# Kernel tuning notes

Hardware: AMD Instinct MI355X
Metric: run time of the kernel (lower is better)

## Reference

```python
import jax, jax.numpy as jnp
import numpy as np

KERNEL = 5
PAD = (KERNEL - 1) // 2  # fixed_padding with dilation=1: pad_beg = pad_end = 2


def setup_inputs() -> dict:
    key = jax.random.key(0)
    kx, kw = jax.random.split(key)
    x = jax.random.normal(kx, (4, 4, 1024, 1024), dtype=jnp.float32)
    weight = jax.random.normal(kw, (4, 4, KERNEL, KERNEL), dtype=jnp.float32)
    return {"x": x, "weight": weight}


def reference(x, weight):
    """Morphological dilation2d: out[b,o,h,w] = max_{c,i,j} (x_pad[b,c,h+i,w+j] + w[o,c,i,j]).

    Equivalent to the torch unfold + broadcast-add + max over dim C*k*k, but computed
    as a fused sliding-window max-plus without materializing the im2col tensor.
    """
    B, C, H, W = x.shape
    k = weight.shape[-1]
    xp = jnp.pad(x, ((0, 0), (0, 0), (PAD, PAD), (PAD, PAD)))  # zero pad, same as F.pad
    out = None
    for i in range(k):
        for j in range(k):
            patch = xp[:, :, i:i + H, j:j + W]          # (B, C, H, W)
            w_ij = weight[:, :, i, j]                    # (O, C)
            # max over in_channels of (x + w) for this tap
            val = jnp.max(patch[:, None] + w_ij[None, :, :, None, None], axis=2)  # (B, O, H, W)
            out = val if out is None else jnp.maximum(out, val)
    return out
```

## Files before the change

### kernel.cpp

```cpp
#include <hip/hip_runtime.h>


constexpr int Himg = 1024, Wimg = 1024, Cin = 4, Cout = 4, Kn = 5;
constexpr int TW = 128, THt = 64;
constexpr int SR = 68;
constexpr int SC4 = 34;
constexpr int S = 140;
constexpr int NCHUNK = SR * SC4;

typedef float v2f __attribute__((ext_vector_type(2)));
typedef const float __attribute__((address_space(4))) cfloat;

__device__ __forceinline__ int rot(int r) { return ((r >> 2) & 1) * 4; }

__global__ __launch_bounds__(256, 4) void morph(const float* __restrict__ x,
                                                const float* __restrict__ w,
                                                float* __restrict__ out) {
  __shared__ __align__(16) float xs[SR * S];
  const int tid = threadIdx.x;
  const int bw = blockIdx.x * TW;
  const int br = blockIdx.y * THt;
  const int b  = blockIdx.z >> 1;
  const int o0 = (blockIdx.z & 1) * 2;
  const int tx = tid & 15;
  const int ty = tid >> 4;
  const int h0 = ty * 4;
  const int w0 = tx * 8;

  cfloat* cw = (cfloat*)w;

  v2f acc[2][4][4];
#pragma unroll
  for (int oo = 0; oo < 2; ++oo)
#pragma unroll
    for (int d = 0; d < 4; ++d)
#pragma unroll
      for (int m = 0; m < 4; ++m) acc[oo][d][m] = (v2f){-3.4e38f, -3.4e38f};

#pragma unroll 1
  for (int c = 0; c < Cin; ++c) {
    if (c) __syncthreads();
    for (int idx = tid; idx < NCHUNK; idx += 256) {
      const int row = idx / SC4;
      const int ch  = idx - row * SC4;
      const int gr  = br - 2 + row;
      const int gc  = bw - 4 + ch * 4;
      float4 v = make_float4(0.f, 0.f, 0.f, 0.f);
      if ((unsigned)gr < (unsigned)Himg) {
        const float* src = x + ((size_t)(b * Cin + c) * Himg + gr) * Wimg;
        if (gc >= 0 && gc <= Wimg - 4) {
          v = *(const float4*)(src + gc);
        } else {
          if ((unsigned)(gc + 0) < (unsigned)Wimg) v.x = src[gc + 0];
          if ((unsigned)(gc + 1) < (unsigned)Wimg) v.y = src[gc + 1];
          if ((unsigned)(gc + 2) < (unsigned)Wimg) v.z = src[gc + 2];
          if ((unsigned)(gc + 3) < (unsigned)Wimg) v.w = src[gc + 3];
        }
      }
      *(float4*)&xs[row * S + rot(row) + ch * 4] = v;
    }
    __syncthreads();

#pragma unroll 1
    for (int rr = 0; rr < 8; ++rr) {
      const int lrow = h0 + rr;
      const float* rb = &xs[lrow * S + rot(lrow) + w0];
      const float4 q0 = *(const float4*)(rb + 0);
      const float4 q1 = *(const float4*)(rb + 4);
      const float4 q2 = *(const float4*)(rb + 8);
      const float4 q3 = *(const float4*)(rb + 12);
      v2f E[6];
      E[0] = (v2f){q0.z, q0.w};
      E[1] = (v2f){q1.x, q1.y};
      E[2] = (v2f){q1.z, q1.w};
      E[3] = (v2f){q2.x, q2.y};
      E[4] = (v2f){q2.z, q2.w};
      E[5] = (v2f){q3.x, q3.y};
      v2f O[5];
      O[0] = (v2f){q0.w, q1.x};
      O[1] = (v2f){q1.y, q1.z};
      O[2] = (v2f){q1.w, q2.x};
      O[3] = (v2f){q2.y, q2.z};
      O[4] = (v2f){q2.w, q3.x};

#pragma unroll
      for (int oo = 0; oo < 2; ++oo) {
#pragma unroll
        for (int d = 0; d < 4; ++d) {
          const int i = rr - d;
          if (i >= 0 && i < Kn) {
            const int wb = (((o0 + oo) * Cin + c) * Kn + i) * Kn;
            const float w_0 = cw[wb + 0];
            const float w_1 = cw[wb + 1];
            const float w_2 = cw[wb + 2];
            const float w_3 = cw[wb + 3];
            const float w_4 = cw[wb + 4];
            const v2f W0 = (v2f){w_0, w_0};
            const v2f W1 = (v2f){w_1, w_1};
            const v2f W2 = (v2f){w_2, w_2};
            const v2f W3 = (v2f){w_3, w_3};
            const v2f W4 = (v2f){w_4, w_4};
#pragma unroll
            for (int m = 0; m < 4; ++m) {
              v2f s0 = E[m + 0] + W0;
              v2f s1 = O[m + 0] + W1;
              v2f s2 = E[m + 1] + W2;
              v2f s3 = O[m + 1] + W3;
              v2f s4 = E[m + 2] + W4;
              v2f a = acc[oo][d][m];
              a.x = fmaxf(fmaxf(fmaxf(s0.x, s1.x), s2.x),
                          fmaxf(fmaxf(s3.x, s4.x), a.x));
              a.y = fmaxf(fmaxf(fmaxf(s0.y, s1.y), s2.y),
                          fmaxf(fmaxf(s3.y, s4.y), a.y));
              acc[oo][d][m] = a;
            }
          }
        }
      }
    }
  }

#pragma unroll
  for (int oo = 0; oo < 2; ++oo) {
#pragma unroll
    for (int d = 0; d < 4; ++d) {
      const int h = br + h0 + d;
      const size_t base =
          ((size_t)(b * Cout + o0 + oo) * Himg + h) * Wimg + bw + w0;
      *(float4*)&out[base + 0] =
          make_float4(acc[oo][d][0].x, acc[oo][d][0].y, acc[oo][d][1].x, acc[oo][d][1].y);
      *(float4*)&out[base + 4] =
          make_float4(acc[oo][d][2].x, acc[oo][d][2].y, acc[oo][d][3].x, acc[oo][d][3].y);
    }
  }
}

extern "C" void kernel_launch(void* const* d_in, const int* in_sizes, int n_in,
                              void* d_out, int out_size, void* d_ws, size_t ws_size,
                              hipStream_t stream) {
  const float* x = (const float*)d_in[0];
  const float* w = (const float*)d_in[1];
  float* out = (float*)d_out;

  dim3 grid(Wimg / TW, Himg / THt, 4 * 2);
  morph<<<grid, dim3(256), 0, stream>>>(x, w, out);
}
```

Measured before the change: 184.5 us.

## Retile morph to 4x8 per-thread outputs with pre-duplicated weight pairs

Each thread now computes a 4-wide by 8-tall strip instead of 8 wide by 4 tall, and the loop over 12 input rows is fully unrolled per output channel, so each LDS row is reused across more output rows. A small pre-kernel writes the weights as duplicated pairs into the workspace so the main kernel can load v2f weights directly from constant memory. Interior blocks skip boundary checks when staging the tile, and the LDS row-rotation padding is removed. The trade-offs are an extra kernel launch, higher register pressure from the full unroll, and possible LDS bank conflicts without the rotation.

```diff
diff --git a/kernel.cpp b/kernel.cpp
--- a/kernel.cpp
+++ b/kernel.cpp
@@ -5,16 +5,25 @@
 constexpr int TW = 128, THt = 64;
 constexpr int SR = 68;
 constexpr int SC4 = 34;
-constexpr int S = 140;
+constexpr int S = 136;
 constexpr int NCHUNK = SR * SC4;
 
 typedef float v2f __attribute__((ext_vector_type(2)));
-typedef const float __attribute__((address_space(4))) cfloat;
+typedef const v2f __attribute__((address_space(4))) cv2f;
 
-__device__ __forceinline__ int rot(int r) { return ((r >> 2) & 1) * 4; }
+__global__ void reorg_w(const float* __restrict__ w, float* __restrict__ wt2) {
+  int idx = threadIdx.x;
+  if (idx < Cout * Cin * Kn * Kn) {
+    float v = w[idx];
+    wt2[2 * idx + 0] = v;
+    wt2[2 * idx + 1] = v;
+  }
+}
 
+template <bool FAST>
 __global__ __launch_bounds__(256, 4) void morph(const float* __restrict__ x,
-                                                const float* __restrict__ w,
+                                                const float* __restrict__ wt2,
+                                                const float* __restrict__ wraw,
                                                 float* __restrict__ out) {
   __shared__ __align__(16) float xs[SR * S];
   const int tid = threadIdx.x;
@@ -22,97 +31,105 @@
   const int br = blockIdx.y * THt;
   const int b  = blockIdx.z >> 1;
   const int o0 = (blockIdx.z & 1) * 2;
-  const int tx = tid & 15;
-  const int ty = tid >> 4;
-  const int h0 = ty * 4;
-  const int w0 = tx * 8;
+  const int tx = tid & 31;
+  const int ty = tid >> 5;
 
-  cfloat* cw = (cfloat*)w;
+  const bool interior = (blockIdx.x > 0) && (blockIdx.x < gridDim.x - 1) &&
+                        (blockIdx.y > 0) && (blockIdx.y < gridDim.y - 1);
 
-  v2f acc[2][4][4];
+  float acc[2][8][4];
 #pragma unroll
   for (int oo = 0; oo < 2; ++oo)
 #pragma unroll
-    for (int d = 0; d < 4; ++d)
+    for (int d = 0; d < 8; ++d)
 #pragma unroll
-      for (int m = 0; m < 4; ++m) acc[oo][d][m] = (v2f){-3.4e38f, -3.4e38f};
+      for (int q = 0; q < 4; ++q) acc[oo][d][q] = -3.4e38f;
 
 #pragma unroll 1
   for (int c = 0; c < Cin; ++c) {
     if (c) __syncthreads();
+    const float* src0 = x + (size_t)(b * Cin + c) * Himg * Wimg;
     for (int idx = tid; idx < NCHUNK; idx += 256) {
       const int row = idx / SC4;
       const int ch  = idx - row * SC4;
       const int gr  = br - 2 + row;
       const int gc  = bw - 4 + ch * 4;
-      float4 v = make_float4(0.f, 0.f, 0.f, 0.f);
-      if ((unsigned)gr < (unsigned)Himg) {
-        const float* src = x + ((size_t)(b * Cin + c) * Himg + gr) * Wimg;
-        if (gc >= 0 && gc <= Wimg - 4) {
-          v = *(const float4*)(src + gc);
-        } else {
-          if ((unsigned)(gc + 0) < (unsigned)Wimg) v.x = src[gc + 0];
-          if ((unsigned)(gc + 1) < (unsigned)Wimg) v.y = src[gc + 1];
-          if ((unsigned)(gc + 2) < (unsigned)Wimg) v.z = src[gc + 2];
-          if ((unsigned)(gc + 3) < (unsigned)Wimg) v.w = src[gc + 3];
+      float4 v;
+      if (interior) {
+        v = *(const float4*)(src0 + (size_t)gr * Wimg + gc);
+      } else {
+        v = make_float4(0.f, 0.f, 0.f, 0.f);
+        if ((unsigned)gr < (unsigned)Himg) {
+          const float* src = src0 + (size_t)gr * Wimg;
+          if (gc >= 0 && gc <= Wimg - 4) {
+            v = *(const float4*)(src + gc);
+          } else {
+            if ((unsigned)(gc + 0) < (unsigned)Wimg) v.x = src[gc + 0];
+            if ((unsigned)(gc + 1) < (unsigned)Wimg) v.y = src[gc + 1];
+            if ((unsigned)(gc + 2) < (unsigned)Wimg) v.z = src[gc + 2];
+            if ((unsigned)(gc + 3) < (unsigned)Wimg) v.w = src[gc + 3];
+          }
         }
       }
-      *(float4*)&xs[row * S + rot(row) + ch * 4] = v;
+      *(float4*)&xs[row * S + ch * 4] = v;
     }
     __syncthreads();
 
-#pragma unroll 1
-    for (int rr = 0; rr < 8; ++rr) {
-      const int lrow = h0 + rr;
-      const float* rb = &xs[lrow * S + rot(lrow) + w0];
-      const float4 q0 = *(const float4*)(rb + 0);
-      const float4 q1 = *(const float4*)(rb + 4);
-      const float4 q2 = *(const float4*)(rb + 8);
-      const float4 q3 = *(const float4*)(rb + 12);
-      v2f E[6];
-      E[0] = (v2f){q0.z, q0.w};
-      E[1] = (v2f){q1.x, q1.y};
-      E[2] = (v2f){q1.z, q1.w};
-      E[3] = (v2f){q2.x, q2.y};
-      E[4] = (v2f){q2.z, q2.w};
-      E[5] = (v2f){q3.x, q3.y};
-      v2f O[5];
-      O[0] = (v2f){q0.w, q1.x};
-      O[1] = (v2f){q1.y, q1.z};
-      O[2] = (v2f){q1.w, q2.x};
-      O[3] = (v2f){q2.y, q2.z};
-      O[4] = (v2f){q2.w, q3.x};
+#pragma unroll
+    for (int oo = 0; oo < 2; ++oo) {
+      const int wb = ((o0 + oo) * Cin + c) * (Kn * Kn);
+      cv2f* W = (cv2f*)wt2 + wb;
+      const float* wr = wraw + wb;
 
 #pragma unroll
-      for (int oo = 0; oo < 2; ++oo) {
+      for (int rr = 0; rr < 12; ++rr) {
+        const float* rb = &xs[(ty * 8 + rr) * S + tx * 4];
+        const float4 q0 = *(const float4*)(rb + 0);
+        const float4 q1 = *(const float4*)(rb + 4);
+        const float4 q2 = *(const float4*)(rb + 8);
+        v2f P[7];
+        P[0] = (v2f){q0.z, q0.w};
+        P[1] = (v2f){q0.w, q1.x};
+        P[2] = (v2f){q1.x, q1.y};
+        P[3] = (v2f){q1.y, q1.z};
+        P[4] = (v2f){q1.z, q1.w};
+        P[5] = (v2f){q1.w, q2.x};
+        P[6] = (v2f){q2.x, q2.y};
+
 #pragma unroll
-        for (int d = 0; d < 4; ++d) {
-          const int i = rr - d;
-          if (i >= 0 && i < Kn) {
-            const int wb = (((o0 + oo) * Cin + c) * Kn + i) * Kn;
-            const float w_0 = cw[wb + 0];
-            const float w_1 = cw[wb + 1];
-            const float w_2 = cw[wb + 2];
-            const float w_3 = cw[wb + 3];
-            const float w_4 = cw[wb + 4];
-            const v2f W0 = (v2f){w_0, w_0};
-            const v2f W1 = (v2f){w_1, w_1};
-            const v2f W2 = (v2f){w_2, w_2};
-            const v2f W3 = (v2f){w_3, w_3};
-            const v2f W4 = (v2f){w_4, w_4};
+        for (int i = 0; i < Kn; ++i) {
+          const int d = rr - i;
+          if (d >= 0 && d < 8) {
+            v2f w0, w1, w2, w3, w4;
+            if (FAST) {
+              w0 = W[i * Kn + 0];
+              w1 = W[i * Kn + 1];
+              w2 = W[i * Kn + 2];
+              w3 = W[i * Kn + 3];
+              w4 = W[i * Kn + 4];
+            } else {
+              float s0 = wr[i * Kn + 0], s1 = wr[i * Kn + 1], s2 = wr[i * Kn + 2];
+              float s3 = wr[i * Kn + 3], s4 = wr[i * Kn + 4];
+              w0 = (v2f){s0, s0}; w1 = (v2f){s1, s1}; w2 = (v2f){s2, s2};
+              w3 = (v2f){s3, s3}; w4 = (v2f){s4, s4};
+            }
 #pragma unroll
-            for (int m = 0; m < 4; ++m) {
-              v2f s0 = E[m + 0] + W0;
-              v2f s1 = O[m + 0] + W1;
-              v2f s2 = E[m + 1] + W2;
-              v2f s3 = O[m + 1] + W3;
-              v2f s4 = E[m + 2] + W4;
-              v2f a = acc[oo][d][m];
-              a.x = fmaxf(fmaxf(fmaxf(s0.x, s1.x), s2.x),
-                          fmaxf(fmaxf(s3.x, s4.x), a.x));
-              a.y = fmaxf(fmaxf(fmaxf(s0.y, s1.y), s2.y),
-                          fmaxf(fmaxf(s3.y, s4.y), a.y));
-              acc[oo][d][m] = a;
+            for (int m = 0; m < 2; ++m) {
+              v2f v0 = P[2 * m + 0] + w0;
+              v2f v1 = P[2 * m + 1] + w1;
+              v2f v2_ = P[2 * m + 2] + w2;
+              v2f v3 = P[2 * m + 3] + w3;
+              v2f v4 = P[2 * m + 4] + w4;
+              float a0 = acc[oo][d][2 * m + 0];
+              float a1 = acc[oo][d][2 * m + 1];
+              a0 = fmaxf(fmaxf(a0, v0.x), v1.x);
+              a0 = fmaxf(fmaxf(a0, v2_.x), v3.x);
+              a0 = fmaxf(a0, v4.x);
+              a1 = fmaxf(fmaxf(a1, v0.y), v1.y);
+              a1 = fmaxf(fmaxf(a1, v2_.y), v3.y);
+              a1 = fmaxf(a1, v4.y);
+              acc[oo][d][2 * m + 0] = a0;
+              acc[oo][d][2 * m + 1] = a1;
             }
           }
         }
@@ -123,14 +140,11 @@
 #pragma unroll
   for (int oo = 0; oo < 2; ++oo) {
 #pragma unroll
-    for (int d = 0; d < 4; ++d) {
-      const int h = br + h0 + d;
-      const size_t base =
-          ((size_t)(b * Cout + o0 + oo) * Himg + h) * Wimg + bw + w0;
-      *(float4*)&out[base + 0] =
-          make_float4(acc[oo][d][0].x, acc[oo][d][0].y, acc[oo][d][1].x, acc[oo][d][1].y);
-      *(float4*)&out[base + 4] =
-          make_float4(acc[oo][d][2].x, acc[oo][d][2].y, acc[oo][d][3].x, acc[oo][d][3].y);
+    for (int d = 0; d < 8; ++d) {
+      const int h = br + ty * 8 + d;
+      float4 res = make_float4(acc[oo][d][0], acc[oo][d][1],
+                               acc[oo][d][2], acc[oo][d][3]);
+      *(float4*)&out[((size_t)(b * Cout + o0 + oo) * Himg + h) * Wimg + bw + tx * 4] = res;
     }
   }
 }
@@ -143,5 +157,12 @@
   float* out = (float*)d_out;
 
   dim3 grid(Wimg / TW, Himg / THt, 4 * 2);
-  morph<<<grid, dim3(256), 0, stream>>>(x, w, out);
+
+  if (ws_size >= sizeof(float) * 2 * Cout * Cin * Kn * Kn) {
+    float* wt2 = (float*)d_ws;
+    reorg_w<<<dim3(1), dim3(512), 0, stream>>>(w, wt2);
+    morph<true><<<grid, dim3(256), 0, stream>>>(x, wt2, w, out);
+  } else {
+    morph<false><<<grid, dim3(256), 0, stream>>>(x, nullptr, w, out);
+  }
 }
```

After: 310.3 us. +68.1%, slower.
